# Kernel optimization log

Hardware: AMD Instinct MI355X
Metric: run time of the kernel (lower is better)

Reference implementation:

```python
import jax, jax.numpy as jnp
import numpy as np

NUM_HEADS = 16
HEAD_DIM = 128
WINDOW = 512
ROPE_BASE = 10000.0


def _rope_tables(seq_len, head_dim, dtype=jnp.float32):
    # rotate_dim == head_dim (rope_proportion=1.0)
    inv_freq = 1.0 / (ROPE_BASE ** (jnp.arange(0, head_dim, 2, dtype=jnp.float32) / head_dim))
    freqs = jnp.arange(seq_len, dtype=jnp.float32)[:, None] * inv_freq[None, :]  # (S, D/2)
    return jnp.cos(freqs).astype(dtype), jnp.sin(freqs).astype(dtype)


def _apply_rope(x, cos, sin):
    # x: (B, H, S, D); interleaved-pair RoPE matching torch reference
    x1 = x[..., 0::2]
    x2 = x[..., 1::2]
    cos = cos[None, None]  # (1,1,S,D/2)
    sin = sin[None, None]
    re = x1 * cos - x2 * sin
    ro = x1 * sin + x2 * cos
    out = jnp.stack([re, ro], axis=-1)  # (B,H,S,D/2,2)
    return out.reshape(x.shape)


def setup_inputs() -> dict:
    key = jax.random.key(0)
    ks = jax.random.split(key, 5)
    B, S, D = 2, 2048, 2048
    std = 0.02
    x = jax.random.normal(ks[0], (B, S, D), dtype=jnp.float32)
    Wq = std * jax.random.normal(ks[1], (D, D), dtype=jnp.float32)
    Wk = std * jax.random.normal(ks[2], (D, D), dtype=jnp.float32)
    Wv = std * jax.random.normal(ks[3], (D, D), dtype=jnp.float32)
    Wo = std * jax.random.normal(ks[4], (D, D), dtype=jnp.float32)
    return {"x": x, "Wq": Wq, "Wk": Wk, "Wv": Wv, "Wo": Wo}


def reference(x, Wq, Wk, Wv, Wo):
    B, S, D = x.shape
    H, Dh = NUM_HEADS, HEAD_DIM
    scale = Dh ** -0.5

    def to_heads(t):
        return t.reshape(B, S, H, Dh).transpose(0, 2, 1, 3)  # (B,H,S,Dh)

    q = to_heads(x @ Wq.T)
    k = to_heads(x @ Wk.T)
    v = to_heads(x @ Wv.T)

    cos, sin = _rope_tables(S, Dh)
    q = _apply_rope(q, cos, sin)
    k = _apply_rope(k, cos, sin)

    # sliding-window causal mask: keep if 0 <= row-col < WINDOW
    pos = jnp.arange(S)
    diff = pos[:, None] - pos[None, :]
    keep = (diff >= 0) & (diff < WINDOW)  # (S,S) bool

    scores = jnp.einsum('bhsd,bhtd->bhst', q, k) * scale
    scores = jnp.where(keep[None, None], scores, jnp.finfo(scores.dtype).min)
    attn = jax.nn.softmax(scores, axis=-1)
    out = jnp.einsum('bhst,bhtd->bhsd', attn, v)  # (B,H,S,Dh)
    out = out.transpose(0, 2, 1, 3).reshape(B, S, D)
    return out @ Wo.T
```

## Files before the change

### kernel.cpp

```cpp
#include <hip/hip_runtime.h>
#include <cstdint>
#include <cstddef>

typedef __bf16 bf16x8 __attribute__((ext_vector_type(8)));
typedef float f32x4 __attribute__((ext_vector_type(4)));
typedef float f32x16 __attribute__((ext_vector_type(16)));
typedef unsigned int u32x2v __attribute__((ext_vector_type(2)));
typedef unsigned short u16;

constexpr int S_LEN  = 2048;
constexpr int DMODEL = 2048;
constexpr int NHEAD  = 16;
constexpr int HDIM   = 128;
constexpr int WIN    = 512;

__device__ __forceinline__ u16 f2bf(float f) {
  union { float ff; uint32_t u; } a; a.ff = f;
  return (u16)((a.u + 0x7fffu + ((a.u >> 16) & 1u)) >> 16);
}

__device__ __forceinline__ uint32_t cvtpk(float lo, float hi) {
  uint32_t r;
  asm("v_cvt_pk_bf16_f32 %0, %1, %2" : "=v"(r) : "v"(lo), "v"(hi));
  return r;
}

__global__ void cvt_all(const float* __restrict__ x,  const float* __restrict__ wq,
                        const float* __restrict__ wk, const float* __restrict__ wv,
                        const float* __restrict__ wo,
                        u16* __restrict__ xb,  u16* __restrict__ wqb,
                        u16* __restrict__ wkb, u16* __restrict__ wvb,
                        u16* __restrict__ wob) {
  const int total = 6291456;
  int i = blockIdx.x * blockDim.x + threadIdx.x;
  const int stride = gridDim.x * blockDim.x;
  for (; i < total; i += stride) {
    const int r = i >> 20;
    const float* src; u16* dst; int off;
    if (r < 2)       { src = x;  dst = xb;  off = i; }
    else if (r == 2) { src = wq; dst = wqb; off = i - (2 << 20); }
    else if (r == 3) { src = wk; dst = wkb; off = i - (3 << 20); }
    else if (r == 4) { src = wv; dst = wvb; off = i - (4 << 20); }
    else             { src = wo; dst = wob; off = i - (5 << 20); }
    float4 v = reinterpret_cast<const float4*>(src)[off];
    uint2 pk;
    pk.x = (uint32_t)f2bf(v.x) | ((uint32_t)f2bf(v.y) << 16);
    pk.y = (uint32_t)f2bf(v.z) | ((uint32_t)f2bf(v.w) << 16);
    reinterpret_cast<uint2*>(dst)[off] = pk;
  }
}

__global__ void rope_kernel(float* __restrict__ rc, float* __restrict__ rs) {
  const int i = blockIdx.x * blockDim.x + threadIdx.x;
  const int s = i >> 6, f = i & 63;
  const double inv = exp(-(double)f * (log(10000.0) / 64.0));
  const double a = (double)s * inv;
  rc[i] = (float)cos(a);
  rs[i] = (float)sin(a);
}

__global__ __launch_bounds__(256, 2)
void gemm_qkv(const u16* __restrict__ A,
              const u16* __restrict__ wqb, const u16* __restrict__ wkb,
              const u16* __restrict__ wvb,
              u16* __restrict__ qout, u16* __restrict__ kout, u16* __restrict__ vtout,
              const float* __restrict__ rc, const float* __restrict__ rs) {
  constexpr int K = DMODEL;
  constexpr int BK = 64;
  __shared__ __align__(16) u16 As[128 * BK];
  __shared__ __align__(16) u16 Bs[128 * BK];
  const int region = blockIdx.x >> 4;
  const u16* Bw = region == 0 ? wqb : region == 1 ? wkb : wvb;
  const int tid = threadIdx.x;
  const int w = tid >> 6, lane = tid & 63;
  const int lr = lane & 15, lk = lane >> 4;
  const int wm = w >> 1, wn = w & 1;
  const int brow = blockIdx.y * 128;
  const int bcol = (blockIdx.x & 15) * 128;

  f32x4 acc[4][4] = {};

  const int st_row = w * 32 + (lane >> 3);
  const int st_col = (lane & 7) * 8;
  const u16* Ag = A  + (size_t)(brow + st_row) * K + st_col;
  const u16* Bg = Bw + (size_t)(bcol + st_row) * K + st_col;
  u16* AsW = As + w * 32 * BK;
  u16* BsW = Bs + w * 32 * BK;

  for (int k0 = 0; k0 < K; k0 += BK) {
#pragma unroll
    for (int i = 0; i < 4; ++i)
      __builtin_amdgcn_global_load_lds(
          (const __attribute__((address_space(1))) void*)(Ag + (size_t)i * 8 * K + k0),
          (__attribute__((address_space(3))) void*)(AsW + i * 8 * BK), 16, 0, 0);
#pragma unroll
    for (int i = 0; i < 4; ++i)
      __builtin_amdgcn_global_load_lds(
          (const __attribute__((address_space(1))) void*)(Bg + (size_t)i * 8 * K + k0),
          (__attribute__((address_space(3))) void*)(BsW + i * 8 * BK), 16, 0, 0);
    __syncthreads();
#pragma unroll
    for (int kc = 0; kc < 2; ++kc) {
      bf16x8 a[4], b[4];
#pragma unroll
      for (int m = 0; m < 4; ++m)
        a[m] = *reinterpret_cast<const bf16x8*>(&As[(wm * 64 + m * 16 + lr) * BK + kc * 32 + lk * 8]);
#pragma unroll
      for (int n = 0; n < 4; ++n)
        b[n] = *reinterpret_cast<const bf16x8*>(&Bs[(wn * 64 + n * 16 + lr) * BK + kc * 32 + lk * 8]);
#pragma unroll
      for (int m = 0; m < 4; ++m)
#pragma unroll
        for (int n = 0; n < 4; ++n)
          acc[m][n] = __builtin_amdgcn_mfma_f32_16x16x32_bf16(a[m], b[n], acc[m][n], 0, 0, 0);
    }
    __syncthreads();
  }

  if (region == 2) {
#pragma unroll
    for (int m = 0; m < 4; ++m) {
      const int gm0 = brow + wm * 64 + m * 16 + lk * 4;
      const int b = gm0 >> 11, s = gm0 & 2047;
#pragma unroll
      for (int n = 0; n < 4; ++n) {
        const int gn = bcol + wn * 64 + n * 16 + lr;
        const int h = gn >> 7, dh = gn & 127;
        uint2 pk;
        pk.x = (uint32_t)f2bf(acc[m][n][0]) | ((uint32_t)f2bf(acc[m][n][1]) << 16);
        pk.y = (uint32_t)f2bf(acc[m][n][2]) | ((uint32_t)f2bf(acc[m][n][3]) << 16);
        *reinterpret_cast<uint2*>(&vtout[((size_t)((b * NHEAD + h) * HDIM + dh)) * S_LEN + s]) = pk;
      }
    }
  } else {
    u16* QK = region == 0 ? qout : kout;
#pragma unroll
    for (int m = 0; m < 4; ++m) {
      const int gm0 = brow + wm * 64 + m * 16 + lk * 4;
      const int b = gm0 >> 11, s0 = gm0 & 2047;
#pragma unroll
      for (int n = 0; n < 4; ++n) {
        const int gn = bcol + wn * 64 + n * 16 + lr;
        const int h = gn >> 7, dh = gn & 127;
        const int fi = dh >> 1;
        const bool ev = (dh & 1) == 0;
#pragma unroll
        for (int j = 0; j < 4; ++j) {
          float v = acc[m][n][j];
          float pp = __shfl_xor(v, 1, 64);
          const float c  = rc[(s0 + j) * 64 + fi];
          const float sn = rs[(s0 + j) * 64 + fi];
          float oo = ev ? (v * c - pp * sn) : (pp * sn + v * c);
          if (region == 0) oo *= 0.08838834764831845f;
          QK[((size_t)(b * NHEAD + h) * S_LEN + (s0 + j)) * HDIM + dh] = f2bf(oo);
        }
      }
    }
  }
}

__global__ __launch_bounds__(256, 2)
void gemm_o(const u16* __restrict__ A, const u16* __restrict__ Bw,
            float* __restrict__ O) {
  constexpr int K = DMODEL;
  constexpr int BK = 64;
  __shared__ __align__(16) u16 As[128 * BK];
  __shared__ __align__(16) u16 Bs[128 * BK];
  const int tid = threadIdx.x;
  const int w = tid >> 6, lane = tid & 63;
  const int lr = lane & 15, lk = lane >> 4;
  const int wm = w >> 1, wn = w & 1;
  const int brow = blockIdx.y * 128;
  const int bcol = blockIdx.x * 128;

  f32x4 acc[4][4] = {};

  const int st_row = w * 32 + (lane >> 3);
  const int st_col = (lane & 7) * 8;
  const u16* Ag = A  + (size_t)(brow + st_row) * K + st_col;
  const u16* Bg = Bw + (size_t)(bcol + st_row) * K + st_col;
  u16* AsW = As + w * 32 * BK;
  u16* BsW = Bs + w * 32 * BK;

  for (int k0 = 0; k0 < K; k0 += BK) {
#pragma unroll
    for (int i = 0; i < 4; ++i)
      __builtin_amdgcn_global_load_lds(
          (const __attribute__((address_space(1))) void*)(Ag + (size_t)i * 8 * K + k0),
          (__attribute__((address_space(3))) void*)(AsW + i * 8 * BK), 16, 0, 0);
#pragma unroll
    for (int i = 0; i < 4; ++i)
      __builtin_amdgcn_global_load_lds(
          (const __attribute__((address_space(1))) void*)(Bg + (size_t)i * 8 * K + k0),
          (__attribute__((address_space(3))) void*)(BsW + i * 8 * BK), 16, 0, 0);
    __syncthreads();
#pragma unroll
    for (int kc = 0; kc < 2; ++kc) {
      bf16x8 a[4], b[4];
#pragma unroll
      for (int m = 0; m < 4; ++m)
        a[m] = *reinterpret_cast<const bf16x8*>(&As[(wm * 64 + m * 16 + lr) * BK + kc * 32 + lk * 8]);
#pragma unroll
      for (int n = 0; n < 4; ++n)
        b[n] = *reinterpret_cast<const bf16x8*>(&Bs[(wn * 64 + n * 16 + lr) * BK + kc * 32 + lk * 8]);
#pragma unroll
      for (int m = 0; m < 4; ++m)
#pragma unroll
        for (int n = 0; n < 4; ++n)
          acc[m][n] = __builtin_amdgcn_mfma_f32_16x16x32_bf16(a[m], b[n], acc[m][n], 0, 0, 0);
    }
    __syncthreads();
  }

#pragma unroll
  for (int m = 0; m < 4; ++m) {
    const int gm0 = brow + wm * 64 + m * 16 + lk * 4;
#pragma unroll
    for (int n = 0; n < 4; ++n) {
      const int gn = bcol + wn * 64 + n * 16 + lr;
#pragma unroll
      for (int j = 0; j < 4; ++j)
        O[(size_t)(gm0 + j) * DMODEL + gn] = acc[m][n][j];
    }
  }
}

__global__ __launch_bounds__(256, 2)
void swa3_kernel(const u16* __restrict__ Qp, const u16* __restrict__ Kp,
                 const u16* __restrict__ Vt, u16* __restrict__ AO) {
  __shared__ __align__(16) u16 Ksh[2][64 * 128];
  __shared__ __align__(16) u16 Vsh[2][128 * 64];

  const int lin = blockIdx.x + gridDim.x * blockIdx.y;
  const int slot = lin >> 3;
  const int bh = (lin & 7) * 4 + (slot >> 4);
  const int qt = slot & 15;

  const int w = threadIdx.x >> 6;
  const int lane = threadIdx.x & 63;
  const int lq = lane & 31, hi = lane >> 5;
  const int qb_blk = qt * 128;
  const int qw = qb_blk + w * 32;
  const int qq = qw + lq;

  const u16* Qb = Qp + (size_t)bh * S_LEN * HDIM;
  const u16* Kb = Kp + (size_t)bh * S_LEN * HDIM;
  const u16* Vb = Vt + (size_t)bh * HDIM * S_LEN;

  bf16x8 qf[8];
#pragma unroll
  for (int s = 0; s < 8; ++s)
    qf[s] = *reinterpret_cast<const bf16x8*>(&Qb[(size_t)qq * HDIM + s * 16 + hi * 8]);

  f32x16 ot[4] = {};
  float m = 0.f, lsum = 0.f;

  const int c_lo = (qb_blk >= WIN) ? qb_blk - WIN : 0;
  const int c_hi = qb_blk + 128;

  auto stage = [&](int buf, int kc) {
#pragma unroll
    for (int i = 0; i < 4; ++i) {
      const int u = i * 256 + w * 64 + lane;
      const int row = u >> 4, sl = (u & 15) ^ (row & 7);
      __builtin_amdgcn_global_load_lds(
          (const __attribute__((address_space(1))) void*)(Kb + (size_t)(kc + row) * HDIM + sl * 8),
          (__attribute__((address_space(3))) void*)(&Ksh[buf][(size_t)(i * 256 + w * 64) * 8]),
          16, 0, 0);
    }
#pragma unroll
    for (int i = 0; i < 4; ++i) {
      const int u = i * 256 + w * 64 + lane;
      const int row = u >> 3, sl = (u & 7) ^ (row & 7);
      __builtin_amdgcn_global_load_lds(
          (const __attribute__((address_space(1))) void*)(Vb + (size_t)row * S_LEN + kc + sl * 8),
          (__attribute__((address_space(3))) void*)(&Vsh[buf][(size_t)(i * 256 + w * 64) * 8]),
          16, 0, 0);
    }
  };

  int buf = 0;
  stage(0, c_lo);
  __syncthreads();

  for (int kc = c_lo; kc < c_hi; kc += 64, buf ^= 1) {
    if (kc + 64 < c_hi) stage(buf ^ 1, kc + 64);

#pragma unroll
    for (int half = 0; half < 2; ++half) {
      const int kch = kc + half * 32;
      if (kch > qw + 31 || kch < qw - 542) continue;

      f32x16 P = {};
#pragma unroll
      for (int s = 0; s < 8; ++s) {
        const int row = half * 32 + lq;
        const int byte = row * 256 + ((s * 32 + hi * 16) ^ ((row & 7) << 4));
        bf16x8 kf = *reinterpret_cast<const bf16x8*>(&Ksh[buf][byte >> 1]);
        P = __builtin_amdgcn_mfma_f32_32x32x16_bf16(kf, qf[s], P, 0, 0, 0);
      }

      const bool needmask = (kch + 32 > qw) || (qw + 31 - kch >= WIN);
      float p[16];
      float pmax = -1e30f;
#pragma unroll
      for (int r = 0; r < 16; ++r) {
        float v = P[r];
        if (needmask) {
          const int kk = kch + (r & 3) + ((r >> 2) << 3) + hi * 4;
          const bool keep = (qq >= kk) && (qq - kk < WIN);
          v = keep ? v : -1e30f;
        }
        p[r] = v;
        pmax = fmaxf(pmax, v);
      }

      if (__any(pmax - m > 8.f)) {
        const float rm = fmaxf(pmax, __shfl_xor(pmax, 32, 64));
        const float mnew = fmaxf(m, rm);
        const float alpha = __expf(m - mnew);
        lsum *= alpha;
#pragma unroll
        for (int dt = 0; dt < 4; ++dt)
#pragma unroll
          for (int r = 0; r < 16; ++r) ot[dt][r] *= alpha;
        m = mnew;
      }

      float ls = 0.f;
#pragma unroll
      for (int r = 0; r < 16; ++r) {
        p[r] = __expf(p[r] - m);
        ls += p[r];
      }
      lsum += ls;

      uint32_t W[8];
#pragma unroll
      for (int i = 0; i < 8; ++i) W[i] = cvtpk(p[2 * i], p[2 * i + 1]);
      u32x2v r02 = __builtin_amdgcn_permlane32_swap(W[0], W[2], false, false);
      u32x2v r13 = __builtin_amdgcn_permlane32_swap(W[1], W[3], false, false);
      u32x2v r46 = __builtin_amdgcn_permlane32_swap(W[4], W[6], false, false);
      u32x2v r57 = __builtin_amdgcn_permlane32_swap(W[5], W[7], false, false);

#pragma unroll
      for (int ks = 0; ks < 2; ++ks) {
        union { uint32_t u[4]; bf16x8 v; } pb;
        if (ks == 0) { pb.u[0] = r02[0]; pb.u[1] = r13[0]; pb.u[2] = r02[1]; pb.u[3] = r13[1]; }
        else         { pb.u[0] = r46[0]; pb.u[1] = r57[0]; pb.u[2] = r46[1]; pb.u[3] = r57[1]; }
#pragma unroll
        for (int dt = 0; dt < 4; ++dt) {
          const int d = dt * 32 + lq;
          const int byte = d * 128 + ((half * 64 + ks * 32 + hi * 16) ^ ((d & 7) << 4));
          bf16x8 vf = *reinterpret_cast<const bf16x8*>(&Vsh[buf][byte >> 1]);
          ot[dt] = __builtin_amdgcn_mfma_f32_32x32x16_bf16(vf, pb.v, ot[dt], 0, 0, 0);
        }
      }
    }
    __syncthreads();
  }

  const float lf = lsum + __shfl_xor(lsum, 32, 64);
  const float inv = 1.f / lf;
  const int b = bh >> 4, h = bh & 15;
  u16* Ob = AO + (size_t)(b * S_LEN + qq) * DMODEL + h * HDIM;
#pragma unroll
  for (int dt = 0; dt < 4; ++dt)
#pragma unroll
    for (int rq = 0; rq < 4; ++rq) {
      uint2 pk;
      pk.x = cvtpk(ot[dt][rq * 4 + 0] * inv, ot[dt][rq * 4 + 1] * inv);
      pk.y = cvtpk(ot[dt][rq * 4 + 2] * inv, ot[dt][rq * 4 + 3] * inv);
      *reinterpret_cast<uint2*>(&Ob[dt * 32 + rq * 8 + hi * 4]) = pk;
    }
}

extern "C" void kernel_launch(void* const* d_in, const int* in_sizes, int n_in,
                              void* d_out, int out_size, void* d_ws, size_t ws_size,
                              hipStream_t stream) {
  const float* x  = (const float*)d_in[0];
  const float* Wq = (const float*)d_in[1];
  const float* Wk = (const float*)d_in[2];
  const float* Wv = (const float*)d_in[3];
  const float* Wo = (const float*)d_in[4];
  float* out = (float*)d_out;

  u16* p = (u16*)d_ws;
  u16* xb  = p; p += (size_t)4096 * 2048;
  u16* wqb = p; p += (size_t)2048 * 2048;
  u16* wkb = p; p += (size_t)2048 * 2048;
  u16* wvb = p; p += (size_t)2048 * 2048;
  u16* wob = p; p += (size_t)2048 * 2048;
  u16* qb  = p; p += (size_t)32 * 2048 * 128;
  u16* kb  = p; p += (size_t)32 * 2048 * 128;
  u16* vtb = p; p += (size_t)32 * 128 * 2048;
  u16* aob = p; p += (size_t)4096 * 2048;
  float* rc = (float*)p;
  float* rs = rc + (size_t)2048 * 64;

  cvt_all<<<3072, 256, 0, stream>>>(x, Wq, Wk, Wv, Wo, xb, wqb, wkb, wvb, wob);
  rope_kernel<<<512, 256, 0, stream>>>(rc, rs);
  gemm_qkv<<<dim3(48, 32), 256, 0, stream>>>(xb, wqb, wkb, wvb, qb, kb, vtb, rc, rs);
  swa3_kernel<<<dim3(16, 32), 256, 0, stream>>>(qb, kb, vtb, aob);
  gemm_o<<<dim3(16, 32), 256, 0, stream>>>(aob, wob, out);
}
```

Before: 228.6 us.

## Replace QKV and output GEMMs with 256-row tiles and a 4-stage async pipeline

Merges the two GEMM kernels into one templated kernel that uses 512 threads and 256x256 (QKV) or 256x128 (output) tiles. Operands are prefetched three k-steps ahead through a 4-slot LDS ring using global_load_lds, with explicit vmcnt waits and split barriers so loads overlap the MFMA work. The kernel also raises wave priority around the MFMA blocks and remaps blocks so that tiles sharing data land on the same XCD. The larger tiles cut global and LDS traffic per FLOP, but they need far more LDS (128 KB for the QKV kernel) and launch fewer blocks, which may hurt occupancy.

```diff
diff --git a/kernel.cpp b/kernel.cpp
--- a/kernel.cpp
+++ b/kernel.cpp
@@ -13,6 +13,12 @@
 constexpr int NHEAD  = 16;
 constexpr int HDIM   = 128;
 constexpr int WIN    = 512;
+
+#define AS1 __attribute__((address_space(1)))
+#define AS3 __attribute__((address_space(3)))
+#define CFENCE asm volatile("" ::: "memory")
+#define BAR() do { CFENCE; __builtin_amdgcn_s_barrier(); CFENCE; } while (0)
+#define WAITVM(n) asm volatile("s_waitcnt vmcnt(" #n ")" ::: "memory")
 
 __device__ __forceinline__ u16 f2bf(float f) {
   union { float ff; uint32_t u; } a; a.ff = f;
@@ -59,94 +65,152 @@
   rs[i] = (float)sin(a);
 }
 
-__global__ __launch_bounds__(256, 2)
-void gemm_qkv(const u16* __restrict__ A,
-              const u16* __restrict__ wqb, const u16* __restrict__ wkb,
-              const u16* __restrict__ wvb,
-              u16* __restrict__ qout, u16* __restrict__ kout, u16* __restrict__ vtout,
-              const float* __restrict__ rc, const float* __restrict__ rs) {
+template<int MODE>
+__global__ __launch_bounds__(512, 2)
+void gemm256(const u16* __restrict__ A,
+             const u16* __restrict__ B0, const u16* __restrict__ B1,
+             const u16* __restrict__ B2,
+             u16* __restrict__ qout, u16* __restrict__ kout, u16* __restrict__ vtout,
+             float* __restrict__ oout,
+             const float* __restrict__ rc, const float* __restrict__ rs) {
   constexpr int K = DMODEL;
-  constexpr int BK = 64;
-  __shared__ __align__(16) u16 As[128 * BK];
-  __shared__ __align__(16) u16 Bs[128 * BK];
-  const int region = blockIdx.x >> 4;
-  const u16* Bw = region == 0 ? wqb : region == 1 ? wkb : wvb;
+  constexpr int NK = K / 32;
+  constexpr int NF = (MODE == 0) ? 4 : 2;
+  constexpr int BSLOT = (MODE == 0) ? 8192 : 4096;
+  constexpr int NBL = (MODE == 0) ? 2 : 1;
+  __shared__ __align__(16) u16 sm[(MODE == 0) ? 65536 : 49152];
+
+  const int lin = blockIdx.x;
+  const int xcd = lin & 7, idx = lin >> 3;
+  int mt, ct;
+  if constexpr (MODE == 0) { mt = idx & 15; ct = xcd * 3 + (idx >> 4); }
+  else                     { mt = idx & 15; ct = xcd * 2 + (idx >> 4); }
+  const int region = (MODE == 0) ? (ct >> 3) : 0;
+  const u16* Bw = (MODE == 0) ? (region == 0 ? B0 : region == 1 ? B1 : B2) : B0;
+  const int brow = mt * 256;
+  const int bcoll = (MODE == 0) ? (ct & 7) * 256 : ct * 128;
+
   const int tid = threadIdx.x;
   const int w = tid >> 6, lane = tid & 63;
   const int lr = lane & 15, lk = lane >> 4;
-  const int wm = w >> 1, wn = w & 1;
-  const int brow = blockIdx.y * 128;
-  const int bcol = (blockIdx.x & 15) * 128;
-
-  f32x4 acc[4][4] = {};
-
-  const int st_row = w * 32 + (lane >> 3);
-  const int st_col = (lane & 7) * 8;
-  const u16* Ag = A  + (size_t)(brow + st_row) * K + st_col;
-  const u16* Bg = Bw + (size_t)(bcol + st_row) * K + st_col;
-  u16* AsW = As + w * 32 * BK;
-  u16* BsW = Bs + w * 32 * BK;
-
-  for (int k0 = 0; k0 < K; k0 += BK) {
-#pragma unroll
-    for (int i = 0; i < 4; ++i)
-      __builtin_amdgcn_global_load_lds(
-          (const __attribute__((address_space(1))) void*)(Ag + (size_t)i * 8 * K + k0),
-          (__attribute__((address_space(3))) void*)(AsW + i * 8 * BK), 16, 0, 0);
-#pragma unroll
-    for (int i = 0; i < 4; ++i)
-      __builtin_amdgcn_global_load_lds(
-          (const __attribute__((address_space(1))) void*)(Bg + (size_t)i * 8 * K + k0),
-          (__attribute__((address_space(3))) void*)(BsW + i * 8 * BK), 16, 0, 0);
-    __syncthreads();
-#pragma unroll
-    for (int kc = 0; kc < 2; ++kc) {
-      bf16x8 a[4], b[4];
-#pragma unroll
-      for (int m = 0; m < 4; ++m)
-        a[m] = *reinterpret_cast<const bf16x8*>(&As[(wm * 64 + m * 16 + lr) * BK + kc * 32 + lk * 8]);
-#pragma unroll
-      for (int n = 0; n < 4; ++n)
-        b[n] = *reinterpret_cast<const bf16x8*>(&Bs[(wn * 64 + n * 16 + lr) * BK + kc * 32 + lk * 8]);
-#pragma unroll
-      for (int m = 0; m < 4; ++m)
-#pragma unroll
-        for (int n = 0; n < 4; ++n)
-          acc[m][n] = __builtin_amdgcn_mfma_f32_16x16x32_bf16(a[m], b[n], acc[m][n], 0, 0, 0);
-    }
-    __syncthreads();
+  const int wm = w >> 2, wn = w & 3;
+
+  const u16* Ag = A  + (size_t)brow * K;
+  const u16* Bg = Bw + (size_t)bcoll * K;
+  u16* Asl = sm;
+  u16* Bsl = sm + 32768;
+
+  f32x4 acc[8][NF] = {};
+
+  auto stageA = [&](int s) {
+    u16* slot = Asl + (s & 3) * 8192;
+#pragma unroll
+    for (int i = 0; i < 2; ++i) {
+      const int MF = i * 8 + w;
+      const u16* src = Ag + (size_t)(MF * 16 + lr) * K + s * 32 + lk * 8;
+      __builtin_amdgcn_global_load_lds((const AS1 void*)src,
+          (AS3 void*)(slot + (i * 512 + w * 64) * 8), 16, 0, 0);
+    }
+  };
+  auto stageB = [&](int s) {
+    u16* slot = Bsl + (s & 3) * BSLOT;
+#pragma unroll
+    for (int i = 0; i < NBL; ++i) {
+      const int MF = i * 8 + w;
+      const u16* src = Bg + (size_t)(MF * 16 + lr) * K + s * 32 + lk * 8;
+      __builtin_amdgcn_global_load_lds((const AS1 void*)src,
+          (AS3 void*)(slot + (i * 512 + w * 64) * 8), 16, 0, 0);
+    }
+  };
+
+#pragma unroll
+  for (int s = 0; s < 3; ++s) { stageA(s); stageB(s); }
+  if constexpr (MODE == 0) WAITVM(8); else WAITVM(6);
+  BAR();
+
+  for (int s = 0; s < NK; ++s) {
+    const u16* As = Asl + (s & 3) * 8192;
+    const u16* Bs = Bsl + (s & 3) * BSLOT;
+    bf16x8 afr[4], bfr[NF];
+#pragma unroll
+    for (int ml = 0; ml < 4; ++ml)
+      afr[ml] = *reinterpret_cast<const bf16x8*>(As + ((wm * 8 + ml) * 64 + lk * 16 + lr) * 8);
+#pragma unroll
+    for (int nf = 0; nf < NF; ++nf)
+      bfr[nf] = *reinterpret_cast<const bf16x8*>(Bs + ((wn * NF + nf) * 64 + lk * 16 + lr) * 8);
+    if (s + 3 < NK) stageA(s + 3);
+    BAR();
+    __builtin_amdgcn_s_setprio(1);
+#pragma unroll
+    for (int ml = 0; ml < 4; ++ml)
+#pragma unroll
+      for (int nf = 0; nf < NF; ++nf)
+        acc[ml][nf] = __builtin_amdgcn_mfma_f32_16x16x32_bf16(afr[ml], bfr[nf], acc[ml][nf], 0, 0, 0);
+    __builtin_amdgcn_s_setprio(0);
+    BAR();
+    bf16x8 afr2[4];
+#pragma unroll
+    for (int ml = 0; ml < 4; ++ml)
+      afr2[ml] = *reinterpret_cast<const bf16x8*>(As + ((wm * 8 + 4 + ml) * 64 + lk * 16 + lr) * 8);
+    if (s + 3 < NK) stageB(s + 3);
+    BAR();
+    __builtin_amdgcn_s_setprio(1);
+#pragma unroll
+    for (int ml = 0; ml < 4; ++ml)
+#pragma unroll
+      for (int nf = 0; nf < NF; ++nf)
+        acc[4 + ml][nf] = __builtin_amdgcn_mfma_f32_16x16x32_bf16(afr2[ml], bfr[nf], acc[4 + ml][nf], 0, 0, 0);
+    __builtin_amdgcn_s_setprio(0);
+    if constexpr (MODE == 0) {
+      if (s < NK - 3) { WAITVM(8); } else if (s == NK - 3) { WAITVM(4); } else if (s == NK - 2) { WAITVM(0); }
+    } else {
+      if (s < NK - 3) { WAITVM(6); } else if (s == NK - 3) { WAITVM(3); } else if (s == NK - 2) { WAITVM(0); }
+    }
+    BAR();
   }
 
-  if (region == 2) {
-#pragma unroll
-    for (int m = 0; m < 4; ++m) {
-      const int gm0 = brow + wm * 64 + m * 16 + lk * 4;
-      const int b = gm0 >> 11, s = gm0 & 2047;
-#pragma unroll
-      for (int n = 0; n < 4; ++n) {
-        const int gn = bcol + wn * 64 + n * 16 + lr;
+  if constexpr (MODE == 1) {
+#pragma unroll
+    for (int mf = 0; mf < 8; ++mf) {
+      const int gm0 = brow + wm * 128 + mf * 16 + lk * 4;
+#pragma unroll
+      for (int nf = 0; nf < NF; ++nf) {
+        const int gn = bcoll + wn * (16 * NF) + nf * 16 + lr;
+#pragma unroll
+        for (int j = 0; j < 4; ++j)
+          oout[(size_t)(gm0 + j) * DMODEL + gn] = acc[mf][nf][j];
+      }
+    }
+  } else if (region == 2) {
+#pragma unroll
+    for (int mf = 0; mf < 8; ++mf) {
+      const int gm0 = brow + wm * 128 + mf * 16 + lk * 4;
+      const int b = gm0 >> 11, s0 = gm0 & 2047;
+#pragma unroll
+      for (int nf = 0; nf < NF; ++nf) {
+        const int gn = bcoll + wn * 64 + nf * 16 + lr;
         const int h = gn >> 7, dh = gn & 127;
         uint2 pk;
-        pk.x = (uint32_t)f2bf(acc[m][n][0]) | ((uint32_t)f2bf(acc[m][n][1]) << 16);
-        pk.y = (uint32_t)f2bf(acc[m][n][2]) | ((uint32_t)f2bf(acc[m][n][3]) << 16);
-        *reinterpret_cast<uint2*>(&vtout[((size_t)((b * NHEAD + h) * HDIM + dh)) * S_LEN + s]) = pk;
+        pk.x = (uint32_t)f2bf(acc[mf][nf][0]) | ((uint32_t)f2bf(acc[mf][nf][1]) << 16);
+        pk.y = (uint32_t)f2bf(acc[mf][nf][2]) | ((uint32_t)f2bf(acc[mf][nf][3]) << 16);
+        *reinterpret_cast<uint2*>(&vtout[((size_t)((b * NHEAD + h) * HDIM + dh)) * S_LEN + s0]) = pk;
       }
     }
   } else {
     u16* QK = region == 0 ? qout : kout;
 #pragma unroll
-    for (int m = 0; m < 4; ++m) {
-      const int gm0 = brow + wm * 64 + m * 16 + lk * 4;
+    for (int mf = 0; mf < 8; ++mf) {
+      const int gm0 = brow + wm * 128 + mf * 16 + lk * 4;
       const int b = gm0 >> 11, s0 = gm0 & 2047;
 #pragma unroll
-      for (int n = 0; n < 4; ++n) {
-        const int gn = bcol + wn * 64 + n * 16 + lr;
+      for (int nf = 0; nf < NF; ++nf) {
+        const int gn = bcoll + wn * 64 + nf * 16 + lr;
         const int h = gn >> 7, dh = gn & 127;
         const int fi = dh >> 1;
         const bool ev = (dh & 1) == 0;
 #pragma unroll
         for (int j = 0; j < 4; ++j) {
-          float v = acc[m][n][j];
+          float v = acc[mf][nf][j];
           float pp = __shfl_xor(v, 1, 64);
           const float c  = rc[(s0 + j) * 64 + fi];
           const float sn = rs[(s0 + j) * 64 + fi];
@@ -160,72 +224,6 @@
 }
 
 __global__ __launch_bounds__(256, 2)
-void gemm_o(const u16* __restrict__ A, const u16* __restrict__ Bw,
-            float* __restrict__ O) {
-  constexpr int K = DMODEL;
-  constexpr int BK = 64;
-  __shared__ __align__(16) u16 As[128 * BK];
-  __shared__ __align__(16) u16 Bs[128 * BK];
-  const int tid = threadIdx.x;
-  const int w = tid >> 6, lane = tid & 63;
-  const int lr = lane & 15, lk = lane >> 4;
-  const int wm = w >> 1, wn = w & 1;
-  const int brow = blockIdx.y * 128;
-  const int bcol = blockIdx.x * 128;
-
-  f32x4 acc[4][4] = {};
-
-  const int st_row = w * 32 + (lane >> 3);
-  const int st_col = (lane & 7) * 8;
-  const u16* Ag = A  + (size_t)(brow + st_row) * K + st_col;
-  const u16* Bg = Bw + (size_t)(bcol + st_row) * K + st_col;
-  u16* AsW = As + w * 32 * BK;
-  u16* BsW = Bs + w * 32 * BK;
-
-  for (int k0 = 0; k0 < K; k0 += BK) {
-#pragma unroll
-    for (int i = 0; i < 4; ++i)
-      __builtin_amdgcn_global_load_lds(
-          (const __attribute__((address_space(1))) void*)(Ag + (size_t)i * 8 * K + k0),
-          (__attribute__((address_space(3))) void*)(AsW + i * 8 * BK), 16, 0, 0);
-#pragma unroll
-    for (int i = 0; i < 4; ++i)
-      __builtin_amdgcn_global_load_lds(
-          (const __attribute__((address_space(1))) void*)(Bg + (size_t)i * 8 * K + k0),
-          (__attribute__((address_space(3))) void*)(BsW + i * 8 * BK), 16, 0, 0);
-    __syncthreads();
-#pragma unroll
-    for (int kc = 0; kc < 2; ++kc) {
-      bf16x8 a[4], b[4];
-#pragma unroll
-      for (int m = 0; m < 4; ++m)
-        a[m] = *reinterpret_cast<const bf16x8*>(&As[(wm * 64 + m * 16 + lr) * BK + kc * 32 + lk * 8]);
-#pragma unroll
-      for (int n = 0; n < 4; ++n)
-        b[n] = *reinterpret_cast<const bf16x8*>(&Bs[(wn * 64 + n * 16 + lr) * BK + kc * 32 + lk * 8]);
-#pragma unroll
-      for (int m = 0; m < 4; ++m)
-#pragma unroll
-        for (int n = 0; n < 4; ++n)
-          acc[m][n] = __builtin_amdgcn_mfma_f32_16x16x32_bf16(a[m], b[n], acc[m][n], 0, 0, 0);
-    }
-    __syncthreads();
-  }
-
-#pragma unroll
-  for (int m = 0; m < 4; ++m) {
-    const int gm0 = brow + wm * 64 + m * 16 + lk * 4;
-#pragma unroll
-    for (int n = 0; n < 4; ++n) {
-      const int gn = bcol + wn * 64 + n * 16 + lr;
-#pragma unroll
-      for (int j = 0; j < 4; ++j)
-        O[(size_t)(gm0 + j) * DMODEL + gn] = acc[m][n][j];
-    }
-  }
-}
-
-__global__ __launch_bounds__(256, 2)
 void swa3_kernel(const u16* __restrict__ Qp, const u16* __restrict__ Kp,
                  const u16* __restrict__ Vt, u16* __restrict__ AO) {
   __shared__ __align__(16) u16 Ksh[2][64 * 128];
@@ -264,18 +262,16 @@
       const int u = i * 256 + w * 64 + lane;
       const int row = u >> 4, sl = (u & 15) ^ (row & 7);
       __builtin_amdgcn_global_load_lds(
-          (const __attribute__((address_space(1))) void*)(Kb + (size_t)(kc + row) * HDIM + sl * 8),
-          (__attribute__((address_space(3))) void*)(&Ksh[buf][(size_t)(i * 256 + w * 64) * 8]),
-          16, 0, 0);
+          (const AS1 void*)(Kb + (size_t)(kc + row) * HDIM + sl * 8),
+          (AS3 void*)(&Ksh[buf][(size_t)(i * 256 + w * 64) * 8]), 16, 0, 0);
     }
 #pragma unroll
     for (int i = 0; i < 4; ++i) {
       const int u = i * 256 + w * 64 + lane;
       const int row = u >> 3, sl = (u & 7) ^ (row & 7);
       __builtin_amdgcn_global_load_lds(
-          (const __attribute__((address_space(1))) void*)(Vb + (size_t)row * S_LEN + kc + sl * 8),
-          (__attribute__((address_space(3))) void*)(&Vsh[buf][(size_t)(i * 256 + w * 64) * 8]),
-          16, 0, 0);
+          (const AS1 void*)(Vb + (size_t)row * S_LEN + kc + sl * 8),
+          (AS3 void*)(&Vsh[buf][(size_t)(i * 256 + w * 64) * 8]), 16, 0, 0);
     }
   };
 
@@ -400,7 +396,7 @@
 
   cvt_all<<<3072, 256, 0, stream>>>(x, Wq, Wk, Wv, Wo, xb, wqb, wkb, wvb, wob);
   rope_kernel<<<512, 256, 0, stream>>>(rc, rs);
-  gemm_qkv<<<dim3(48, 32), 256, 0, stream>>>(xb, wqb, wkb, wvb, qb, kb, vtb, rc, rs);
+  gemm256<0><<<384, 512, 0, stream>>>(xb, wqb, wkb, wvb, qb, kb, vtb, nullptr, rc, rs);
   swa3_kernel<<<dim3(16, 32), 256, 0, stream>>>(qb, kb, vtb, aob);
-  gemm_o<<<dim3(16, 32), 256, 0, stream>>>(aob, wob, out);
-}
+  gemm256<1><<<256, 512, 0, stream>>>(aob, wob, nullptr, nullptr, nullptr, nullptr, nullptr, out, nullptr, nullptr);
+}
```

After: 253.7 us. 11.0% more time.

## Rewrite QKV GEMM with 256x256 tiles, 8 waves, and double-buffered async LDS pipeline

Applied to the files above, without the earlier changes.

The QKV projection GEMM moves from 128x128 tiles with 4 waves and single-buffered LDS to 256x256 tiles with 8 waves. K-tiles are double-buffered and staged in half-slices, interleaved with the MFMA phases using explicit vmcnt waits, raw barriers and setprio. A swizzled block index groups tiles for L2 reuse. The goal is to raise arithmetic intensity and hide global load latency behind compute. The cost is more accumulator registers (128 floats per lane), about 128KB of LDS per block, and a fragile hand-tuned wait/barrier schedule.

```diff
diff --git a/kernel.cpp b/kernel.cpp
--- a/kernel.cpp
+++ b/kernel.cpp
@@ -13,6 +13,11 @@
 constexpr int NHEAD  = 16;
 constexpr int HDIM   = 128;
 constexpr int WIN    = 512;
+
+#define AS1 __attribute__((address_space(1)))
+#define AS3 __attribute__((address_space(3)))
+#define BAR() do { asm volatile("" ::: "memory"); __builtin_amdgcn_s_barrier(); asm volatile("" ::: "memory"); } while (0)
+#define WAITVM(n) asm volatile("s_waitcnt vmcnt(" #n ")" ::: "memory")
 
 __device__ __forceinline__ u16 f2bf(float f) {
   union { float ff; uint32_t u; } a; a.ff = f;
@@ -59,100 +64,153 @@
   rs[i] = (float)sin(a);
 }
 
-__global__ __launch_bounds__(256, 2)
-void gemm_qkv(const u16* __restrict__ A,
-              const u16* __restrict__ wqb, const u16* __restrict__ wkb,
-              const u16* __restrict__ wvb,
-              u16* __restrict__ qout, u16* __restrict__ kout, u16* __restrict__ vtout,
-              const float* __restrict__ rc, const float* __restrict__ rs) {
+__global__ __launch_bounds__(512, 2)
+void gemm_qkv256(const u16* __restrict__ A,
+                 const u16* __restrict__ B0w, const u16* __restrict__ B1w,
+                 const u16* __restrict__ B2w,
+                 u16* __restrict__ qout, u16* __restrict__ kout, u16* __restrict__ vtout,
+                 const float* __restrict__ rc, const float* __restrict__ rs) {
   constexpr int K = DMODEL;
-  constexpr int BK = 64;
-  __shared__ __align__(16) u16 As[128 * BK];
-  __shared__ __align__(16) u16 Bs[128 * BK];
-  const int region = blockIdx.x >> 4;
-  const u16* Bw = region == 0 ? wqb : region == 1 ? wkb : wvb;
+  constexpr int NT = K / 64;
+  __shared__ __align__(16) u16 sm[2][2][16384];
+
+  const int g = (blockIdx.x & 7) * 48 + (blockIdx.x >> 3);
+  const int mt = g / 24, ct = g % 24;
+  const int region = ct >> 3;
+  const u16* Bw = region == 0 ? B0w : region == 1 ? B1w : B2w;
+  const int brow = mt * 256;
+  const int bcoll = (ct & 7) * 256;
+
   const int tid = threadIdx.x;
   const int w = tid >> 6, lane = tid & 63;
   const int lr = lane & 15, lk = lane >> 4;
-  const int wm = w >> 1, wn = w & 1;
-  const int brow = blockIdx.y * 128;
-  const int bcol = (blockIdx.x & 15) * 128;
-
-  f32x4 acc[4][4] = {};
-
-  const int st_row = w * 32 + (lane >> 3);
-  const int st_col = (lane & 7) * 8;
-  const u16* Ag = A  + (size_t)(brow + st_row) * K + st_col;
-  const u16* Bg = Bw + (size_t)(bcol + st_row) * K + st_col;
-  u16* AsW = As + w * 32 * BK;
-  u16* BsW = Bs + w * 32 * BK;
-
-  for (int k0 = 0; k0 < K; k0 += BK) {
-#pragma unroll
-    for (int i = 0; i < 4; ++i)
-      __builtin_amdgcn_global_load_lds(
-          (const __attribute__((address_space(1))) void*)(Ag + (size_t)i * 8 * K + k0),
-          (__attribute__((address_space(3))) void*)(AsW + i * 8 * BK), 16, 0, 0);
-#pragma unroll
-    for (int i = 0; i < 4; ++i)
-      __builtin_amdgcn_global_load_lds(
-          (const __attribute__((address_space(1))) void*)(Bg + (size_t)i * 8 * K + k0),
-          (__attribute__((address_space(3))) void*)(BsW + i * 8 * BK), 16, 0, 0);
-    __syncthreads();
-#pragma unroll
-    for (int kc = 0; kc < 2; ++kc) {
-      bf16x8 a[4], b[4];
-#pragma unroll
-      for (int m = 0; m < 4; ++m)
-        a[m] = *reinterpret_cast<const bf16x8*>(&As[(wm * 64 + m * 16 + lr) * BK + kc * 32 + lk * 8]);
-#pragma unroll
-      for (int n = 0; n < 4; ++n)
-        b[n] = *reinterpret_cast<const bf16x8*>(&Bs[(wn * 64 + n * 16 + lr) * BK + kc * 32 + lk * 8]);
-#pragma unroll
-      for (int m = 0; m < 4; ++m)
-#pragma unroll
-        for (int n = 0; n < 4; ++n)
-          acc[m][n] = __builtin_amdgcn_mfma_f32_16x16x32_bf16(a[m], b[n], acc[m][n], 0, 0, 0);
-    }
-    __syncthreads();
+  const int wm = w >> 2, wn = w & 3;
+
+  const u16* Ag = A  + (size_t)brow * K;
+  const u16* Bg = Bw + (size_t)bcoll * K;
+
+  f32x4 acc[8][4] = {};
+
+  auto stage = [&](int mat, int tt, int h) {
+#pragma unroll
+    for (int i = 0; i < 2; ++i) {
+      const int u = h * 1024 + i * 512 + tid;
+      const int MF = (u >> 6) & 15, lkk = (u >> 4) & 3, lrr = u & 15;
+      const u16* src = (mat == 0 ? Ag : Bg) + (size_t)(MF * 16 + lrr) * K + tt * 64 + h * 32 + lkk * 8;
+      __builtin_amdgcn_global_load_lds((const AS1 void*)src,
+          (AS3 void*)(&sm[tt & 1][mat][(size_t)(h * 1024 + i * 512 + w * 64) * 8]), 16, 0, 0);
+    }
+  };
+
+  stage(0, 0, 0); stage(1, 0, 0);
+  stage(0, 0, 1); stage(1, 0, 1);
+  stage(0, 1, 0); stage(1, 1, 0);
+  WAITVM(8);
+  BAR();
+
+  for (int t = 0; t < NT; ++t) {
+    const u16* Asl = &sm[t & 1][0][0];
+    const u16* Bsl = &sm[t & 1][1][0];
+    bf16x8 a[4], b[4];
+#pragma unroll
+    for (int ml = 0; ml < 4; ++ml)
+      a[ml] = *reinterpret_cast<const bf16x8*>(Asl + (((wm * 8 + ml) * 4 + lk) * 16 + lr) * 8);
+#pragma unroll
+    for (int nf = 0; nf < 4; ++nf)
+      b[nf] = *reinterpret_cast<const bf16x8*>(Bsl + (((wn * 4 + nf) * 4 + lk) * 16 + lr) * 8);
+    if (t + 1 < NT) stage(0, t + 1, 1);
+    BAR();
+    __builtin_amdgcn_s_setprio(1);
+#pragma unroll
+    for (int ml = 0; ml < 4; ++ml)
+#pragma unroll
+      for (int nf = 0; nf < 4; ++nf)
+        acc[ml][nf] = __builtin_amdgcn_mfma_f32_16x16x32_bf16(a[ml], b[nf], acc[ml][nf], 0, 0, 0);
+    __builtin_amdgcn_s_setprio(0);
+    BAR();
+    bf16x8 a2[4];
+#pragma unroll
+    for (int ml = 0; ml < 4; ++ml)
+      a2[ml] = *reinterpret_cast<const bf16x8*>(Asl + (((wm * 8 + 4 + ml) * 4 + lk) * 16 + lr) * 8);
+    if (t + 1 < NT) stage(1, t + 1, 1);
+    BAR();
+    __builtin_amdgcn_s_setprio(1);
+#pragma unroll
+    for (int ml = 0; ml < 4; ++ml)
+#pragma unroll
+      for (int nf = 0; nf < 4; ++nf)
+        acc[4 + ml][nf] = __builtin_amdgcn_mfma_f32_16x16x32_bf16(a2[ml], b[nf], acc[4 + ml][nf], 0, 0, 0);
+    __builtin_amdgcn_s_setprio(0);
+    if (t + 1 < NT) { WAITVM(8); } else { WAITVM(0); }
+    BAR();
+#pragma unroll
+    for (int ml = 0; ml < 4; ++ml)
+      a[ml] = *reinterpret_cast<const bf16x8*>(Asl + ((((16 + wm * 8 + ml) * 4) + lk) * 16 + lr) * 8);
+#pragma unroll
+    for (int nf = 0; nf < 4; ++nf)
+      b[nf] = *reinterpret_cast<const bf16x8*>(Bsl + ((((16 + wn * 4 + nf) * 4) + lk) * 16 + lr) * 8);
+    if (t + 2 < NT) stage(0, t + 2, 0);
+    BAR();
+    __builtin_amdgcn_s_setprio(1);
+#pragma unroll
+    for (int ml = 0; ml < 4; ++ml)
+#pragma unroll
+      for (int nf = 0; nf < 4; ++nf)
+        acc[ml][nf] = __builtin_amdgcn_mfma_f32_16x16x32_bf16(a[ml], b[nf], acc[ml][nf], 0, 0, 0);
+    __builtin_amdgcn_s_setprio(0);
+    BAR();
+#pragma unroll
+    for (int ml = 0; ml < 4; ++ml)
+      a2[ml] = *reinterpret_cast<const bf16x8*>(Asl + ((((16 + wm * 8 + 4 + ml) * 4) + lk) * 16 + lr) * 8);
+    if (t + 2 < NT) stage(1, t + 2, 0);
+    BAR();
+    __builtin_amdgcn_s_setprio(1);
+#pragma unroll
+    for (int ml = 0; ml < 4; ++ml)
+#pragma unroll
+      for (int nf = 0; nf < 4; ++nf)
+        acc[4 + ml][nf] = __builtin_amdgcn_mfma_f32_16x16x32_bf16(a2[ml], b[nf], acc[4 + ml][nf], 0, 0, 0);
+    __builtin_amdgcn_s_setprio(0);
+    if (t + 2 < NT) { WAITVM(8); } else if (t + 2 == NT) { WAITVM(4); }
+    BAR();
   }
 
   if (region == 2) {
 #pragma unroll
-    for (int m = 0; m < 4; ++m) {
-      const int gm0 = brow + wm * 64 + m * 16 + lk * 4;
-      const int b = gm0 >> 11, s = gm0 & 2047;
-#pragma unroll
-      for (int n = 0; n < 4; ++n) {
-        const int gn = bcol + wn * 64 + n * 16 + lr;
+    for (int mf = 0; mf < 8; ++mf) {
+      const int gm0 = brow + wm * 128 + mf * 16 + lk * 4;
+      const int b_ = gm0 >> 11, s0 = gm0 & 2047;
+#pragma unroll
+      for (int nf = 0; nf < 4; ++nf) {
+        const int gn = bcoll + wn * 64 + nf * 16 + lr;
         const int h = gn >> 7, dh = gn & 127;
         uint2 pk;
-        pk.x = (uint32_t)f2bf(acc[m][n][0]) | ((uint32_t)f2bf(acc[m][n][1]) << 16);
-        pk.y = (uint32_t)f2bf(acc[m][n][2]) | ((uint32_t)f2bf(acc[m][n][3]) << 16);
-        *reinterpret_cast<uint2*>(&vtout[((size_t)((b * NHEAD + h) * HDIM + dh)) * S_LEN + s]) = pk;
+        pk.x = (uint32_t)f2bf(acc[mf][nf][0]) | ((uint32_t)f2bf(acc[mf][nf][1]) << 16);
+        pk.y = (uint32_t)f2bf(acc[mf][nf][2]) | ((uint32_t)f2bf(acc[mf][nf][3]) << 16);
+        *reinterpret_cast<uint2*>(&vtout[((size_t)((b_ * NHEAD + h) * HDIM + dh)) * S_LEN + s0]) = pk;
       }
     }
   } else {
     u16* QK = region == 0 ? qout : kout;
 #pragma unroll
-    for (int m = 0; m < 4; ++m) {
-      const int gm0 = brow + wm * 64 + m * 16 + lk * 4;
-      const int b = gm0 >> 11, s0 = gm0 & 2047;
-#pragma unroll
-      for (int n = 0; n < 4; ++n) {
-        const int gn = bcol + wn * 64 + n * 16 + lr;
+    for (int mf = 0; mf < 8; ++mf) {
+      const int gm0 = brow + wm * 128 + mf * 16 + lk * 4;
+      const int b_ = gm0 >> 11, s0 = gm0 & 2047;
+#pragma unroll
+      for (int nf = 0; nf < 4; ++nf) {
+        const int gn = bcoll + wn * 64 + nf * 16 + lr;
         const int h = gn >> 7, dh = gn & 127;
         const int fi = dh >> 1;
         const bool ev = (dh & 1) == 0;
 #pragma unroll
         for (int j = 0; j < 4; ++j) {
-          float v = acc[m][n][j];
+          float v = acc[mf][nf][j];
           float pp = __shfl_xor(v, 1, 64);
           const float c  = rc[(s0 + j) * 64 + fi];
           const float sn = rs[(s0 + j) * 64 + fi];
           float oo = ev ? (v * c - pp * sn) : (pp * sn + v * c);
           if (region == 0) oo *= 0.08838834764831845f;
-          QK[((size_t)(b * NHEAD + h) * S_LEN + (s0 + j)) * HDIM + dh] = f2bf(oo);
+          QK[((size_t)(b_ * NHEAD + h) * S_LEN + (s0 + j)) * HDIM + dh] = f2bf(oo);
         }
       }
     }
@@ -186,13 +244,13 @@
 #pragma unroll
     for (int i = 0; i < 4; ++i)
       __builtin_amdgcn_global_load_lds(
-          (const __attribute__((address_space(1))) void*)(Ag + (size_t)i * 8 * K + k0),
-          (__attribute__((address_space(3))) void*)(AsW + i * 8 * BK), 16, 0, 0);
+          (const AS1 void*)(Ag + (size_t)i * 8 * K + k0),
+          (AS3 void*)(AsW + i * 8 * BK), 16, 0, 0);
 #pragma unroll
     for (int i = 0; i < 4; ++i)
       __builtin_amdgcn_global_load_lds(
-          (const __attribute__((address_space(1))) void*)(Bg + (size_t)i * 8 * K + k0),
-          (__attribute__((address_space(3))) void*)(BsW + i * 8 * BK), 16, 0, 0);
+          (const AS1 void*)(Bg + (size_t)i * 8 * K + k0),
+          (AS3 void*)(BsW + i * 8 * BK), 16, 0, 0);
     __syncthreads();
 #pragma unroll
     for (int kc = 0; kc < 2; ++kc) {
@@ -264,18 +322,16 @@
       const int u = i * 256 + w * 64 + lane;
       const int row = u >> 4, sl = (u & 15) ^ (row & 7);
       __builtin_amdgcn_global_load_lds(
-          (const __attribute__((address_space(1))) void*)(Kb + (size_t)(kc + row) * HDIM + sl * 8),
-          (__attribute__((address_space(3))) void*)(&Ksh[buf][(size_t)(i * 256 + w * 64) * 8]),
-          16, 0, 0);
+          (const AS1 void*)(Kb + (size_t)(kc + row) * HDIM + sl * 8),
+          (AS3 void*)(&Ksh[buf][(size_t)(i * 256 + w * 64) * 8]), 16, 0, 0);
     }
 #pragma unroll
     for (int i = 0; i < 4; ++i) {
       const int u = i * 256 + w * 64 + lane;
       const int row = u >> 3, sl = (u & 7) ^ (row & 7);
       __builtin_amdgcn_global_load_lds(
-          (const __attribute__((address_space(1))) void*)(Vb + (size_t)row * S_LEN + kc + sl * 8),
-          (__attribute__((address_space(3))) void*)(&Vsh[buf][(size_t)(i * 256 + w * 64) * 8]),
-          16, 0, 0);
+          (const AS1 void*)(Vb + (size_t)row * S_LEN + kc + sl * 8),
+          (AS3 void*)(&Vsh[buf][(size_t)(i * 256 + w * 64) * 8]), 16, 0, 0);
     }
   };
 
@@ -400,7 +456,7 @@
 
   cvt_all<<<3072, 256, 0, stream>>>(x, Wq, Wk, Wv, Wo, xb, wqb, wkb, wvb, wob);
   rope_kernel<<<512, 256, 0, stream>>>(rc, rs);
-  gemm_qkv<<<dim3(48, 32), 256, 0, stream>>>(xb, wqb, wkb, wvb, qb, kb, vtb, rc, rs);
+  gemm_qkv256<<<384, 512, 0, stream>>>(xb, wqb, wkb, wvb, qb, kb, vtb, rc, rs);
   swa3_kernel<<<dim3(16, 32), 256, 0, stream>>>(qb, kb, vtb, aob);
   gemm_o<<<dim3(16, 32), 256, 0, stream>>>(aob, wob, out);
 }
```

After: 246.7 us. 1.08x slower.
